# Performance work log

Hardware: AMD Instinct MI355X
Metric: run time of the kernel (lower is better)

Reference implementation:

```python
import jax, jax.numpy as jnp
import numpy as np

T = 22        # TypeEncoder.tensor_size() (assumed)
H = 2         # attention heads
C = 64        # hc_graph (per-head out channels)
L = 3         # num_hops
LEAFCAT = 5   # len(LeafType.valid_categories()) (assumed)
NSIZES = 8    # len(LeafType.valid_sizes()) (assumed)
HL = 64       # hc_linear
HT = 64       # hc_task == hc_leafsize
SLOPE = 0.2   # PyG GATConv negative_slope


def _gat(x, src, dst, W, asrc, adst, b):
    # PyG GATConv (concat=True, dropout=0, self-loops already appended to src/dst)
    N = x.shape[0]
    h = (x @ W).reshape(N, H, C)                      # [N,H,C]
    a_s = jnp.einsum('nhc,hc->nh', h, asrc)            # per-node src score
    a_d = jnp.einsum('nhc,hc->nh', h, adst)            # per-node dst score
    e = jax.nn.leaky_relu(a_s[src] + a_d[dst], SLOPE)  # [E+N,H]
    m = jax.ops.segment_max(e, dst, num_segments=N)
    p = jnp.exp(e - m[dst])
    s = jax.ops.segment_sum(p, dst, num_segments=N)
    alpha = p / (s[dst] + 1e-16)                       # scatter-softmax over in-edges
    out = jax.ops.segment_sum(h[src] * alpha[:, :, None], dst, num_segments=N)
    return out.reshape(N, H * C) + b


def _mlp2(z, W1, b1, W2, b2):
    return jax.nn.relu(z @ W1 + b1) @ W2 + b2


def setup_inputs() -> dict:
    key = jax.random.key(0)
    ks = jax.random.split(key, 32)
    N, E, NG, NPG = 102400, 1228800, 256, 400
    D = H * C
    g = lambda k, shp, fan: (jax.random.normal(k, shp, jnp.float32) / np.sqrt(fan)).astype(jnp.float32)
    z = lambda *shp: jnp.zeros(shp, jnp.float32)
    return {
        'x': jax.random.normal(ks[0], (N, D), jnp.float32),
        'edge_index': jax.random.randint(ks[1], (2, E), 0, N),
        'batch': jnp.repeat(jnp.arange(NG, dtype=jnp.int32), NPG),
        'gat_W': g(ks[2], (L, D, D), D),
        'gat_asrc': g(ks[3], (L, H, C), C),
        'gat_adst': g(ks[4], (L, H, C), C),
        'gat_b': z(L, D),
        'shared_W': g(ks[5], (D + T, HL), D + T),
        'shared_b': z(HL),
        'ptr_W1': g(ks[6], (3, HL, HT), HL), 'ptr_b1': z(3, HT),
        'ptr_W2': g(ks[7], (3, HT, 3), HT), 'ptr_b2': z(3, 3),
        'cat_W1': g(ks[8], (HL, HT), HL), 'cat_b1': z(HT),
        'cat_W2': g(ks[9], (HT, LEAFCAT), HT), 'cat_b2': z(LEAFCAT),
        'sf_W1': g(ks[10], (2, HL, HT), HL), 'sf_b1': z(2, HT),
        'sf_W2': g(ks[11], (2, HT, 1), HT), 'sf_b2': z(2, 1),
        'bool_W1': g(ks[12], (HL + T + LEAFCAT + 2, HT), HL + T + LEAFCAT + 2), 'bool_b1': z(HT),
        'bool_W2': g(ks[13], (HT, 1), HT), 'bool_b2': z(1),
        'size_W1': g(ks[14], (HL + T + LEAFCAT + 3, HT), HL + T + LEAFCAT + 3), 'size_b1': z(HT),
        'size_W2': g(ks[15], (HT, NSIZES), HT), 'size_b2': z(NSIZES),
    }


def reference(x, edge_index, batch, gat_W, gat_asrc, gat_adst, gat_b,
              shared_W, shared_b, ptr_W1, ptr_b1, ptr_W2, ptr_b2,
              cat_W1, cat_b1, cat_W2, cat_b2, sf_W1, sf_b1, sf_W2, sf_b2,
              bool_W1, bool_b1, bool_W2, bool_b2, size_W1, size_b1, size_W2, size_b2):
    N = x.shape[0]
    num_graphs = int(batch[-1]) + 1                    # batch is sorted per-graph ids
    node0 = jnp.searchsorted(batch, jnp.arange(num_graphs))  # first node of each graph
    dtype_vec = x[node0, :T]                           # NodeEncoder.split_node_vec dtype slice
    loops = jnp.arange(N)
    src = jnp.concatenate([edge_index[0], loops])      # GATConv add_self_loops=True
    dst = jnp.concatenate([edge_index[1], loops])
    h = x
    for l in range(L):
        h = _gat(h, src, dst, gat_W[l], gat_asrc[l], gat_adst[l], gat_b[l])
        if l < L - 1:
            h = jax.nn.relu(h)
    zf = jax.nn.relu(jnp.concatenate([h[node0], dtype_vec], axis=1) @ shared_W + shared_b)
    # 3 pointer heads, batched
    p = jax.nn.relu(jnp.einsum('gh,khd->kgd', zf, ptr_W1) + ptr_b1[:, None, :])
    ptr = jnp.einsum('kgd,kdo->kgo', p, ptr_W2) + ptr_b2[:, None, :]
    cat_logits = _mlp2(zf, cat_W1, cat_b1, cat_W2, cat_b2)
    q = jax.nn.relu(jnp.einsum('gh,khd->kgd', zf, sf_W1) + sf_b1[:, None, :])
    sf = jnp.einsum('kgd,kdo->kgo', q, sf_W2) + sf_b2[:, None, :]
    signed, floating = sf[0], sf[1]
    bool_in = jnp.concatenate([zf, dtype_vec, cat_logits, signed, floating], axis=1)
    bool_logit = _mlp2(bool_in, bool_W1, bool_b1, bool_W2, bool_b2)
    size_in = jnp.concatenate([bool_in, bool_logit], axis=1)
    size_logits = _mlp2(size_in, size_W1, size_b1, size_W2, size_b2)
    return (ptr[0], ptr[1], ptr[2], cat_logits, signed, floating, bool_logit, size_logits)
```

## Files before the change

### kernel.cpp

```cpp
#include <hip/hip_runtime.h>
#include <hip/hip_bf16.h>

typedef __hip_bfloat16 bf16;
typedef __attribute__((ext_vector_type(8))) short short8;
typedef __attribute__((ext_vector_type(4))) float floatx4;

#define MF(a, b, c) __builtin_amdgcn_mfma_f32_16x16x32_bf16(a, b, c, 0, 0, 0)

__device__ __forceinline__ float b2f(bf16 v) { return __bfloat162float(v); }
__device__ __forceinline__ unsigned short f2us(float f) {
    bf16 h = __float2bfloat16(f);
    return *(unsigned short*)&h;
}
__device__ __forceinline__ float lo2f(unsigned hv) { return __uint_as_float(hv << 16); }
__device__ __forceinline__ float hi2f(unsigned hv) { return __uint_as_float(hv & 0xffff0000u); }
__device__ __forceinline__ float leaky(float v) { return v > 0.f ? v : 0.2f * v; }

__device__ __forceinline__ float ldw(const void* p, size_t i, int f32) {
    return f32 ? ((const float*)p)[i] : b2f(((const bf16*)p)[i]);
}

template <int F32>
__device__ __forceinline__ float LDWt(const void* p, size_t i) {
    return F32 ? ((const float*)p)[i] : b2f(((const bf16*)p)[i]);
}

__device__ __forceinline__ int or16(const int* f) {
    int r = 0;
#pragma unroll
    for (int j = 0; j < 16; j++) r |= f[j];
    return r;
}

__device__ __forceinline__ void quadred(float part[4]) {
#pragma unroll
    for (int m = 1; m <= 8; m <<= 1)
#pragma unroll
        for (int r = 0; r < 4; r++) part[r] += __shfl_xor(part[r], m);
}

__global__ void k_detect_zero(const void* x, int* flagv, char* zbase, size_t zbytes) {
    int b = blockIdx.x;
    int t = threadIdx.x;
    if (b < 16) {
        __shared__ int sbad;
        if (t == 0) sbad = 0;
        __syncthreads();
        float v = b2f(((const bf16*)x)[b * 256 + t]);
        if (!(fabsf(v) < 1e10f)) sbad = 1;
        __syncthreads();
        if (t == 0) flagv[b] = sbad;
    } else {
        size_t off = (size_t)(b - 16) * 4096 + (size_t)t * 16;
        if (off < zbytes) *(uint4*)(zbase + off) = make_uint4(0u, 0u, 0u, 0u);
    }
}

__global__ void k_prep_fused(const void* __restrict__ x, unsigned short* __restrict__ Ab,
                             int nvec,
                             const void* __restrict__ gw, unsigned short* __restrict__ Wt,
                             const void* as_, const void* ad_, const void* b_,
                             float* asF, float* adF, float* bF,
                             const void* sW_, const void* pW1_, const void* cW1_,
                             const void* fW1_, const void* bW1_, const void* zW1_,
                             unsigned short* __restrict__ Whd,
                             const int* __restrict__ batch, int* __restrict__ node0,
                             unsigned char* __restrict__ rootb,
                             unsigned char* __restrict__ flag2, int N,
                             const int* __restrict__ flagv, int nbx8) {
    int b = blockIdx.x;
    int t = threadIdx.x;
    int f32 = or16(flagv);
    if (b < nbx8) {
        int i = b * 256 + t;
        if (i < nvec) {
            if (!f32) {
                ((uint4*)Ab)[i] = ((const uint4*)x)[i];
            } else {
                float4 a = ((const float4*)x)[2 * i];
                float4 c = ((const float4*)x)[2 * i + 1];
                uint4 o;
                o.x = ((unsigned)f2us(a.y) << 16) | f2us(a.x);
                o.y = ((unsigned)f2us(a.w) << 16) | f2us(a.z);
                o.z = ((unsigned)f2us(c.y) << 16) | f2us(c.x);
                o.w = ((unsigned)f2us(c.w) << 16) | f2us(c.z);
                ((uint4*)Ab)[i] = o;
            }
        }
    } else if (b < nbx8 + 192) {
        int i = (b - nbx8) * 256 + t;
        int l = i >> 14, rem = i & 16383, n = rem >> 7, k = rem & 127;
        Wt[i] = f2us(ldw(gw, (size_t)l * 16384 + (size_t)k * 128 + n, f32));
    } else if (b < nbx8 + 194) {
        int i = (b - nbx8 - 192) * 256 + t;
        if (i < 384) {
            asF[i] = ldw(as_, i, f32);
            adF[i] = ldw(ad_, i, f32);
            bF[i] = ldw(b_, i, f32);
        }
    } else if (b < nbx8 + 194 + 184) {
        int i = (b - nbx8 - 194) * 256 + t;
        float v;
        if (i < 10240) {
            int n = i / 160, k = i - n * 160;
            v = (k < 150) ? ldw(sW_, (size_t)k * 64 + n, f32) : 0.f;
        } else if (i < 22528) {
            int j = i - 10240;
            int kk = j >> 12, r = j & 4095, n = r >> 6, k = r & 63;
            v = ldw(pW1_, (size_t)kk * 4096 + (size_t)k * 64 + n, f32);
        } else if (i < 26624) {
            int j = i - 22528;
            int n = j >> 6, k = j & 63;
            v = ldw(cW1_, (size_t)k * 64 + n, f32);
        } else if (i < 34816) {
            int j = i - 26624;
            int kk = j >> 12, r = j & 4095, n = r >> 6, k = r & 63;
            v = ldw(fW1_, (size_t)kk * 4096 + (size_t)k * 64 + n, f32);
        } else if (i < 40960) {
            int j = i - 34816;
            int n = j / 96, k = j - n * 96;
            v = (k < 93) ? ldw(bW1_, (size_t)k * 64 + n, f32) : 0.f;
        } else {
            int j = i - 40960;
            int n = j / 96, k = j - n * 96;
            v = (k < 94) ? ldw(zW1_, (size_t)k * 64 + n, f32) : 0.f;
        }
        Whd[i] = f2us(v);
    } else {
        int i = (b - nbx8 - 194 - 184) * 256 + t;
        if (i < N) {
            int bb = batch[i];
            if (i == 0 || batch[i - 1] != bb) {
                node0[bb] = i;
                rootb[i] = 1;
                flag2[i] = 1;
            }
        }
    }
}

__global__ void k_scan3x(const int* __restrict__ counts,
                         const unsigned char* __restrict__ flag1,
                         const unsigned char* __restrict__ flag2,
                         int* __restrict__ offs, int* __restrict__ wp1, int* __restrict__ wp2,
                         int* __restrict__ bsums, int n) {
    __shared__ int s[256];
    int tid = threadIdx.x;
    int i = blockIdx.x * 256 + tid;
#pragma unroll
    for (int a = 0; a < 3; a++) {
        int v = 0;
        if (i < n) v = (a == 0) ? counts[i] : (a == 1) ? (int)flag1[i] : (int)flag2[i];
        s[tid] = v;
        __syncthreads();
        for (int d = 1; d < 256; d <<= 1) {
            int t2 = (tid >= d) ? s[tid - d] : 0;
            __syncthreads();
            s[tid] += t2;
            __syncthreads();
        }
        int incl = s[tid];
        if (i < n) {
            if (a == 0) offs[i] = incl - v;
            else if (a == 1) wp1[i] = incl - v;
            else wp2[i] = incl - v;
        }
        if (tid == 255) bsums[a * 512 + blockIdx.x] = incl;
        __syncthreads();
    }
}

__global__ void k_scan2x(int* __restrict__ bsums, int nb, int* __restrict__ nact) {
    __shared__ int s[512];
    int tid = threadIdx.x;
#pragma unroll
    for (int a = 0; a < 3; a++) {
        int* arr = bsums + a * 512;
        int v = (tid < nb) ? arr[tid] : 0;
        s[tid] = v;
        __syncthreads();
        for (int d = 1; d < 512; d <<= 1) {
            int t2 = (tid >= d) ? s[tid - d] : 0;
            __syncthreads();
            s[tid] += t2;
            __syncthreads();
        }
        arr[tid] = s[tid] - v;
        if (a >= 1 && tid == 511) nact[a - 1] = s[511];
        __syncthreads();
    }
}

__global__ void k_mark1(const int* __restrict__ ei, const unsigned char* __restrict__ flag2,
                        unsigned char* __restrict__ flag1, int E, int N, int eBlocks) {
    int b = blockIdx.x;
    if (b < eBlocks) {
        int e = b * 256 + threadIdx.x;
        if (e < E && flag2[ei[E + e]]) flag1[ei[e]] = 1;
    } else {
        int i = (b - eBlocks) * 256 + threadIdx.x;
        if (i < N && flag2[i]) flag1[i] = 1;
    }
}

__global__ void k_hist_masked(const int* __restrict__ ei, const unsigned char* __restrict__ flag1,
                              int* __restrict__ counts, int E) {
    int e = blockIdx.x * blockDim.x + threadIdx.x;
    if (e < E) {
        int d = ei[E + e];
        if (flag1[d]) atomicAdd(&counts[d], 1);
    }
}

__global__ void k_scatter_wl(const int* __restrict__ ei, const int* __restrict__ offs,
                             const int* __restrict__ bsums, int* __restrict__ cur,
                             const unsigned char* __restrict__ flag1,
                             const unsigned char* __restrict__ flag2,
                             const int* __restrict__ wp1, const int* __restrict__ wp2,
                             int* __restrict__ adj, int* __restrict__ wl1, int* __restrict__ wl2,
                             int E, int N, int eBlocks) {
    int b = blockIdx.x;
    if (b < eBlocks) {
        int e = b * 256 + threadIdx.x;
        if (e >= E) return;
        int d = ei[E + e];
        if (!flag1[d]) return;
        int r = atomicAdd(&cur[d], 1);
        adj[offs[d] + bsums[d >> 8] + r] = ei[e];
    } else {
        int i = (b - eBlocks) * 256 + threadIdx.x;
        if (i < N) {
            if (flag1[i]) wl1[wp1[i] + bsums[512 + (i >> 8)]] = i;
            if (flag2[i]) wl2[wp2[i] + bsums[1024 + (i >> 8)]] = i;
        }
    }
}

__device__ __forceinline__ void gemm_body(
    const unsigned short* __restrict__ Ab, const unsigned short* __restrict__ Wt,
    unsigned short* __restrict__ Bb, float4* __restrict__ asadv,
    const float* __restrict__ asF, const float* __restrict__ adF, int N,
    const int* __restrict__ wl, const int* __restrict__ nactp, int bb) {
    __shared__ __align__(16) unsigned short Ws[128 * 136];
    __shared__ __align__(16) unsigned short Cs[64 * 136];

    int t = threadIdx.x;
    int r0 = bb * 64;
    int nact = wl ? *nactp : N;
    if (r0 >= nact) return;

    {
        const uint4* src = (const uint4*)Wt;
#pragma unroll
        for (int k = 0; k < 8; k++) {
            int j = t + k * 256;
            int row = j >> 4, c16 = j & 15;
            *(uint4*)&Ws[row * 136 + c16 * 8] = src[j];
        }
    }
    __syncthreads();

    int lane = t & 63;
    int w = t >> 6;
    int ln = lane & 15;
    int quad = lane >> 4;

    int idx = r0 + w * 16 + ln;
    bool valid = idx < nact;
    int arow = idx < N ? idx : N - 1;
    if (wl) arow = valid ? wl[idx] : 0;
    bool wave_active = __any((int)valid);

    if (wave_active) {
        const unsigned short* ap = Ab + (size_t)arow * 128 + quad * 8;

        short8 afrag[4];
        if (valid) {
#pragma unroll
            for (int kt = 0; kt < 4; kt++)
                afrag[kt] = *(const short8*)(ap + kt * 32);
        } else {
#pragma unroll
            for (int kt = 0; kt < 4; kt++)
                afrag[kt] = (short8){0, 0, 0, 0, 0, 0, 0, 0};
        }

        floatx4 acc[8];
#pragma unroll
        for (int nt = 0; nt < 8; nt++) acc[nt] = (floatx4){0.f, 0.f, 0.f, 0.f};

#pragma unroll
        for (int nt = 0; nt < 8; nt++) {
            const unsigned short* wp = Ws + (nt * 16 + ln) * 136 + quad * 8;
#pragma unroll
            for (int kt = 0; kt < 4; kt++) {
                short8 bfrag = *(const short8*)(wp + kt * 32);
                acc[nt] = MF(afrag[kt], bfrag, acc[nt]);
            }
        }

        float as0[4] = {0, 0, 0, 0}, as1[4] = {0, 0, 0, 0};
        float ad0[4] = {0, 0, 0, 0}, ad1[4] = {0, 0, 0, 0};
#pragma unroll
        for (int nt = 0; nt < 8; nt++) {
            float asc = asF[nt * 16 + ln];
            float adc = adF[nt * 16 + ln];
#pragma unroll
            for (int r = 0; r < 4; r++) {
                float v = acc[nt][r];
                Cs[(w * 16 + quad * 4 + r) * 136 + nt * 16 + ln] = f2us(v);
                if (nt < 4) { as0[r] += v * asc; ad0[r] += v * adc; }
                else        { as1[r] += v * asc; ad1[r] += v * adc; }
            }
        }
#pragma unroll
        for (int mask = 1; mask <= 8; mask <<= 1) {
#pragma unroll
            for (int r = 0; r < 4; r++) {
                as0[r] += __shfl_xor(as0[r], mask);
                as1[r] += __shfl_xor(as1[r], mask);
                ad0[r] += __shfl_xor(ad0[r], mask);
                ad1[r] += __shfl_xor(ad1[r], mask);
            }
        }
        if (ln == 0) {
#pragma unroll
            for (int r = 0; r < 4; r++) {
                int idx3 = r0 + w * 16 + quad * 4 + r;
                if (idx3 < nact) {
                    int row = wl ? wl[idx3] : idx3;
                    asadv[row] = make_float4(as0[r], as1[r], ad0[r], ad1[r]);
                }
            }
        }
    }
    __syncthreads();

    {
        int idx2 = r0 + (t >> 2);
        int cseg = (t & 3) * 32;
        if (idx2 < nact) {
            int grow = wl ? wl[idx2] : idx2;
            const short8* srcp = (const short8*)&Cs[(t >> 2) * 136 + cseg];
            short8* dstp = (short8*)&Bb[(size_t)grow * 128 + cseg];
#pragma unroll
            for (int u = 0; u < 4; u++) dstp[u] = srcp[u];
        }
    }
}

__global__ __launch_bounds__(256) void k_gemm_mfma(
    const unsigned short* __restrict__ Ab, const unsigned short* __restrict__ Wt,
    unsigned short* __restrict__ Bb, float4* __restrict__ asadv,
    const float* __restrict__ asF, const float* __restrict__ adF, int N,
    const int* __restrict__ wl, const int* __restrict__ nactp) {
    gemm_body(Ab, Wt, Bb, asadv, asF, adF, N, wl, nactp, blockIdx.x);
}

__global__ __launch_bounds__(256) void k_gemm0_mark(
    const unsigned short* __restrict__ Ab, const unsigned short* __restrict__ Wt,
    unsigned short* __restrict__ Bb, float4* __restrict__ asadv,
    const float* __restrict__ asF, const float* __restrict__ adF, int N,
    const int* __restrict__ ei, const unsigned char* __restrict__ rootb,
    unsigned char* __restrict__ flag2, int E, int markBlocks) {
    int b = blockIdx.x;
    if (b < markBlocks) {
        int e = b * 256 + threadIdx.x;
        if (e < E) {
            int d = ei[E + e];
            if (rootb[d]) flag2[ei[e]] = 1;
        }
        return;
    }
    gemm_body(Ab, Wt, Bb, asadv, asF, adF, N, nullptr, nullptr, b - markBlocks);
}

__global__ void k_gat_agg(const uint2* __restrict__ Bu2, const float4* __restrict__ asadv,
                          const int* __restrict__ offs, const int* __restrict__ bsums,
                          const int* __restrict__ counts,
                          const int* __restrict__ adj, const float* __restrict__ biasF,
                          uint2* __restrict__ Au2, float2* __restrict__ pE,
                          const int* __restrict__ nactp, int nfix, int dorelu, int byidx,
                          const int* __restrict__ wl) {
    int wave = (blockIdx.x * blockDim.x + threadIdx.x) >> 6;
    int lane = threadIdx.x & 63;
    int hl = lane & 31;
    int hb = lane & 32;
    int idx = wave * 2 + (lane >> 5);
    int n = nfix ? nfix : *nactp;
    if (idx >= n) return;
    int node = wl[idx];
    int head = hl >> 4;

    float4 self = asadv[node];
    float ad0 = self.z, ad1 = self.w;
    float es0 = __expf(leaky(self.x + ad0));
    float es1 = __expf(leaky(self.y + ad1));

    int o = offs[node] + bsums[node >> 8];
    int c = counts[node];
    uint2 hvs = Bu2[(size_t)node * 32 + hl];
    float acc0, acc1, acc2, acc3;

    if (c <= 32) {
        int src_r = 0;
        float p0 = 0.f, p1 = 0.f;
        if (hl < c) {
            src_r = adj[o + hl];
            float4 av = asadv[src_r];
            p0 = __expf(leaky(av.x + ad0));
            p1 = __expf(leaky(av.y + ad1));
        }
        float t0 = p0, t1 = p1;
#pragma unroll
        for (int mask = 1; mask <= 16; mask <<= 1) {
            t0 += __shfl_xor(t0, mask);
            t1 += __shfl_xor(t1, mask);
        }
        float inv0 = 1.f / (es0 + t0 + 1e-16f);
        float inv1 = 1.f / (es1 + t1 + 1e-16f);
        p0 *= inv0;
        p1 *= inv1;
        float aself = head ? es1 * inv1 : es0 * inv0;
        acc0 = aself * lo2f(hvs.x);
        acc1 = aself * hi2f(hvs.x);
        acc2 = aself * lo2f(hvs.y);
        acc3 = aself * hi2f(hvs.y);

        uint2 hq[4];
#pragma unroll
        for (int j = 0; j < 4; j++) {
            int s2 = __shfl(src_r, hb + j);
            hq[j] = make_uint2(0u, 0u);
            if (j < c) hq[j] = Bu2[(size_t)s2 * 32 + hl];
        }

        for (int base = 0; base < c; base += 4) {
            uint2 cu[4];
            float av4[4];
#pragma unroll
            for (int j = 0; j < 4; j++) {
                cu[j] = hq[j];
                int idx2 = (base + j) & 31;
                float a0 = __shfl(p0, hb + idx2);
                float a1 = __shfl(p1, hb + idx2);
                float a = head ? a1 : a0;
                av4[j] = (base + j < c) ? a : 0.f;
            }
#pragma unroll
            for (int j = 0; j < 4; j++) {
                int nx = base + 4 + j;
                int s2 = __shfl(src_r, hb + (nx & 31));
                if (nx < c) hq[j] = Bu2[(size_t)s2 * 32 + hl];
            }
#pragma unroll
            for (int j = 0; j < 4; j++) {
                acc0 += av4[j] * lo2f(cu[j].x);
                acc1 += av4[j] * hi2f(cu[j].x);
                acc2 += av4[j] * lo2f(cu[j].y);
                acc3 += av4[j] * hi2f(cu[j].y);
            }
        }
    } else {
        float sum0 = es0, sum1 = es1;
        for (int base = 0; base < c; base += 32) {
            int i = base + hl;
            float p0 = 0.f, p1 = 0.f;
            if (i < c) {
                int s = adj[o + i];
                float4 av = asadv[s];
                p0 = __expf(leaky(av.x + ad0));
                p1 = __expf(leaky(av.y + ad1));
                pE[o + i] = make_float2(p0, p1);
            }
            float t0 = p0, t1 = p1;
#pragma unroll
            for (int mask = 1; mask <= 16; mask <<= 1) {
                t0 += __shfl_xor(t0, mask);
                t1 += __shfl_xor(t1, mask);
            }
            sum0 += t0; sum1 += t1;
        }
        float inv0 = 1.f / (sum0 + 1e-16f);
        float inv1 = 1.f / (sum1 + 1e-16f);
        float aself = head ? es1 * inv1 : es0 * inv0;
        float invh = head ? inv1 : inv0;
        acc0 = aself * lo2f(hvs.x);
        acc1 = aself * hi2f(hvs.x);
        acc2 = aself * lo2f(hvs.y);
        acc3 = aself * hi2f(hvs.y);
        for (int i = 0; i < c; i++) {
            int s = adj[o + i];
            float2 pp = pE[o + i];
            uint2 hv = Bu2[(size_t)s * 32 + hl];
            float a = (head ? pp.y : pp.x) * invh;
            acc0 += a * lo2f(hv.x);
            acc1 += a * hi2f(hv.x);
            acc2 += a * lo2f(hv.y);
            acc3 += a * hi2f(hv.y);
        }
    }

    float4 bb4 = ((const float4*)biasF)[hl];
    float q0 = acc0 + bb4.x;
    float q1 = acc1 + bb4.y;
    float q2 = acc2 + bb4.z;
    float q3 = acc3 + bb4.w;
    if (dorelu) {
        q0 = fmaxf(q0, 0.f); q1 = fmaxf(q1, 0.f);
        q2 = fmaxf(q2, 0.f); q3 = fmaxf(q3, 0.f);
    }
    Au2[(size_t)(byidx ? idx : node) * 32 + hl] =
        make_uint2(((unsigned)f2us(q1) << 16) | f2us(q0),
                   ((unsigned)f2us(q3) << 16) | f2us(q2));
}

template <int F32>
__device__ void heads_mfma_body(
    const unsigned* __restrict__ hroot32, const void* __restrict__ x,
    const int* __restrict__ node0, const unsigned short* __restrict__ Whd,
    const void* sb, const void* pb1, const void* pW2, const void* pb2,
    const void* cb1, const void* cW2, const void* cb2,
    const void* fb1, const void* fW2, const void* fb2,
    const void* bb1, const void* bW2, const void* bb2,
    const void* zb1, const void* zW2, const void* zb2,
    void* __restrict__ outv) {
    __shared__ __align__(16) unsigned short hinS[64 * 168];
    __shared__ __align__(16) unsigned short TwS[4][16 * 168];

    int t = threadIdx.x;
    int g0b = blockIdx.x * 64;
    bf16* outb = (bf16*)outv;
    float* outf = (float*)outv;
#define STORE(idx, val) do { if (F32) outf[idx] = (val); else outb[idx] = __float2bfloat16(val); } while (0)

    {
        unsigned* h32 = (unsigned*)hinS;
        for (int j = t; j < 64 * 64; j += 256) {
            int gl = j >> 6, c = j & 63;
            h32[gl * 84 + c] = hroot32[(size_t)(g0b + gl) * 64 + c];
        }
        for (int j = t; j < 64 * 20; j += 256) {
            int gl = j / 20, c = j - gl * 20;
            int n0 = node0[g0b + gl];
            int k0 = 2 * c;
            float d0 = (k0 < 22) ? LDWt<F32>(x, (size_t)n0 * 128 + k0) : 0.f;
            float d1 = (k0 + 1 < 22) ? LDWt<F32>(x, (size_t)n0 * 128 + k0 + 1) : 0.f;
            h32[gl * 84 + 64 + c] = ((unsigned)f2us(d1) << 16) | f2us(d0);
        }
    }
    __syncthreads();

    int w = t >> 6;
    int lane = t & 63;
    int ln = lane & 15, quad = lane >> 4;
    unsigned short* T = TwS[w];
    int gq = quad * 4;
    int gw0 = g0b + w * 16;

    for (int j = lane; j < 16 * 32; j += 64) {
        int gl = j >> 5, c = j & 31;
        T[gl * 168 + 64 + c] =
            (c < 22) ? hinS[(w * 16 + gl) * 168 + 128 + c] : (unsigned short)0;
    }

    short8 afA[5];
#pragma unroll
    for (int kt = 0; kt < 5; kt++)
        afA[kt] = *(const short8*)&hinS[(w * 16 + ln) * 168 + quad * 8 + kt * 32];
#pragma unroll
    for (int nt = 0; nt < 4; nt++) {
        floatx4 acc = (floatx4){0.f, 0.f, 0.f, 0.f};
        const unsigned short* bp = Whd + (nt * 16 + ln) * 160 + quad * 8;
#pragma unroll
        for (int kt = 0; kt < 5; kt++)
            acc = MF(afA[kt], *(const short8*)(bp + kt * 32), acc);
        float bias = LDWt<F32>(sb, nt * 16 + ln);
#pragma unroll
        for (int r = 0; r < 4; r++)
            T[(gq + r) * 168 + nt * 16 + ln] = f2us(fmaxf(acc[r] + bias, 0.f));
    }
    __syncthreads();

    short8 af20 = *(const short8*)&T[ln * 168 + quad * 8];
    short8 af21 = *(const short8*)&T[ln * 168 + quad * 8 + 32];

#pragma unroll
    for (int k = 0; k < 3; k++) {
        const unsigned short* Bw = Whd + 10240 + k * 4096;
        floatx4 acc[4];
#pragma unroll
        for (int nt = 0; nt < 4; nt++) {
            floatx4 a = (floatx4){0.f, 0.f, 0.f, 0.f};
            const unsigned short* bp = Bw + (nt * 16 + ln) * 64 + quad * 8;
            a = MF(af20, *(const short8*)bp, a);
            a = MF(af21, *(const short8*)(bp + 32), a);
            float b1 = LDWt<F32>(pb1, k * 64 + nt * 16 + ln);
#pragma unroll
            for (int r = 0; r < 4; r++) a[r] = fmaxf(a[r] + b1, 0.f);
            acc[nt] = a;
        }
#pragma unroll
        for (int o = 0; o < 3; o++) {
            float w2[4], part[4];
#pragma unroll
            for (int nt = 0; nt < 4; nt++)
                w2[nt] = LDWt<F32>(pW2, (size_t)k * 192 + (size_t)(nt * 16 + ln) * 3 + o);
#pragma unroll
            for (int r = 0; r < 4; r++)
                part[r] = acc[0][r] * w2[0] + acc[1][r] * w2[1] +
                          acc[2][r] * w2[2] + acc[3][r] * w2[3];
            quadred(part);
            if (ln == 0) {
                float b2 = LDWt<F32>(pb2, k * 3 + o);
#pragma unroll
                for (int r = 0; r < 4; r++)
                    STORE(k * 768 + (gw0 + gq + r) * 3 + o, part[r] + b2);
            }
        }
    }

    {
        const unsigned short* Bw = Whd + 22528;
        floatx4 acc[4];
#pragma unroll
        for (int nt = 0; nt < 4; nt++) {
            floatx4 a = (floatx4){0.f, 0.f, 0.f, 0.f};
            const unsigned short* bp = Bw + (nt * 16 + ln) * 64 + quad * 8;
            a = MF(af20, *(const short8*)bp, a);
            a = MF(af21, *(const short8*)(bp + 32), a);
            float b1 = LDWt<F32>(cb1, nt * 16 + ln);
#pragma unroll
            for (int r = 0; r < 4; r++) a[r] = fmaxf(a[r] + b1, 0.f);
            acc[nt] = a;
        }
#pragma unroll
        for (int o = 0; o < 5; o++) {
            float w2[4], part[4];
#pragma unroll
            for (int nt = 0; nt < 4; nt++)
                w2[nt] = LDWt<F32>(cW2, (size_t)(nt * 16 + ln) * 5 + o);
#pragma unroll
            for (int r = 0; r < 4; r++)
                part[r] = acc[0][r] * w2[0] + acc[1][r] * w2[1] +
                          acc[2][r] * w2[2] + acc[3][r] * w2[3];
            quadred(part);
            if (ln == 0) {
                float b2 = LDWt<F32>(cb2, o);
#pragma unroll
                for (int r = 0; r < 4; r++) {
                    float v = part[r] + b2;
                    T[(gq + r) * 168 + 86 + o] = f2us(v);
                    STORE(2304 + (gw0 + gq + r) * 5 + o, v);
                }
            }
        }
    }

#pragma unroll
    for (int k = 0; k < 2; k++) {
        const unsigned short* Bw = Whd + 26624 + k * 4096;
        floatx4 acc[4];
#pragma unroll
        for (int nt = 0; nt < 4; nt++) {
            floatx4 a = (floatx4){0.f, 0.f, 0.f, 0.f};
            const unsigned short* bp = Bw + (nt * 16 + ln) * 64 + quad * 8;
            a = MF(af20, *(const short8*)bp, a);
            a = MF(af21, *(const short8*)(bp + 32), a);
            float b1 = LDWt<F32>(fb1, k * 64 + nt * 16 + ln);
#pragma unroll
            for (int r = 0; r < 4; r++) a[r] = fmaxf(a[r] + b1, 0.f);
            acc[nt] = a;
        }
        float w2[4], part[4];
#pragma unroll
        for (int nt = 0; nt < 4; nt++)
            w2[nt] = LDWt<F32>(fW2, (size_t)k * 64 + nt * 16 + ln);
#pragma unroll
        for (int r = 0; r < 4; r++)
            part[r] = acc[0][r] * w2[0] + acc[1][r] * w2[1] +
                      acc[2][r] * w2[2] + acc[3][r] * w2[3];
        quadred(part);
        if (ln == 0) {
            float b2 = LDWt<F32>(fb2, k);
#pragma unroll
            for (int r = 0; r < 4; r++) {
                float v = part[r] + b2;
                T[(gq + r) * 168 + 91 + k] = f2us(v);
                STORE(3584 + k * 256 + (gw0 + gq + r), v);
            }
        }
    }
    __syncthreads();

    short8 af3 = *(const short8*)&T[ln * 168 + 64 + quad * 8];

    {
        const unsigned short* Bw = Whd + 34816;
        floatx4 acc[4];
#pragma unroll
        for (int nt = 0; nt < 4; nt++) {
            floatx4 a = (floatx4){0.f, 0.f, 0.f, 0.f};
            const unsigned short* bp = Bw + (nt * 16 + ln) * 96 + quad * 8;
            a = MF(af20, *(const short8*)bp, a);
            a = MF(af21, *(const short8*)(bp + 32), a);
            a = MF(af3, *(const short8*)(bp + 64), a);
            float b1 = LDWt<F32>(bb1, nt * 16 + ln);
#pragma unroll
            for (int r = 0; r < 4; r++) a[r] = fmaxf(a[r] + b1, 0.f);
            acc[nt] = a;
        }
        float w2[4], part[4];
#pragma unroll
        for (int nt = 0; nt < 4; nt++)
            w2[nt] = LDWt<F32>(bW2, nt * 16 + ln);
#pragma unroll
        for (int r = 0; r < 4; r++)
            part[r] = acc[0][r] * w2[0] + acc[1][r] * w2[1] +
                      acc[2][r] * w2[2] + acc[3][r] * w2[3];
        quadred(part);
        if (ln == 0) {
            float b2 = LDWt<F32>(bb2, 0);
#pragma unroll
            for (int r = 0; r < 4; r++) {
                float v = part[r] + b2;
                T[(gq + r) * 168 + 93] = f2us(v);
                STORE(4096 + (gw0 + gq + r), v);
            }
        }
    }
    __syncthreads();

    af3 = *(const short8*)&T[ln * 168 + 64 + quad * 8];

    {
        const unsigned short* Bw = Whd + 40960;
        floatx4 acc[4];
#pragma unroll
        for (int nt = 0; nt < 4; nt++) {
            floatx4 a = (floatx4){0.f, 0.f, 0.f, 0.f};
            const unsigned short* bp = Bw + (nt * 16 + ln) * 96 + quad * 8;
            a = MF(af20, *(const short8*)bp, a);
            a = MF(af21, *(const short8*)(bp + 32), a);
            a = MF(af3, *(const short8*)(bp + 64), a);
            float b1 = LDWt<F32>(zb1, nt * 16 + ln);
#pragma unroll
            for (int r = 0; r < 4; r++) a[r] = fmaxf(a[r] + b1, 0.f);
            acc[nt] = a;
        }
#pragma unroll
        for (int o = 0; o < 8; o++) {
            float w2[4], part[4];
#pragma unroll
            for (int nt = 0; nt < 4; nt++)
                w2[nt] = LDWt<F32>(zW2, (size_t)(nt * 16 + ln) * 8 + o);
#pragma unroll
            for (int r = 0; r < 4; r++)
                part[r] = acc[0][r] * w2[0] + acc[1][r] * w2[1] +
                          acc[2][r] * w2[2] + acc[3][r] * w2[3];
            quadred(part);
            if (ln == 0) {
                float b2 = LDWt<F32>(zb2, o);
#pragma unroll
                for (int r = 0; r < 4; r++)
                    STORE(4352 + (gw0 + gq + r) * 8 + o, part[r] + b2);
            }
        }
    }
#undef STORE
}

__global__ __launch_bounds__(256) void k_heads_mfma(
    const unsigned* __restrict__ hroot32, const void* __restrict__ x,
    const int* __restrict__ node0, const unsigned short* __restrict__ Whd,
    const void* sb, const void* pb1, const void* pW2, const void* pb2,
    const void* cb1, const void* cW2, const void* cb2,
    const void* fb1, const void* fW2, const void* fb2,
    const void* bb1, const void* bW2, const void* bb2,
    const void* zb1, const void* zW2, const void* zb2,
    void* __restrict__ outv, const int* __restrict__ flagv) {
    if (or16(flagv))
        heads_mfma_body<1>(hroot32, x, node0, Whd, sb, pb1, pW2, pb2, cb1, cW2, cb2,
                           fb1, fW2, fb2, bb1, bW2, bb2, zb1, zW2, zb2, outv);
    else
        heads_mfma_body<0>(hroot32, x, node0, Whd, sb, pb1, pW2, pb2, cb1, cW2, cb2,
                           fb1, fW2, fb2, bb1, bW2, bb2, zb1, zW2, zb2, outv);
}


extern "C" void kernel_launch(void* const* d_in, const int* in_sizes, int n_in,
                              void* d_out, int out_size, void* d_ws, size_t ws_size,
                              hipStream_t stream) {
    const void* x     = d_in[0];
    const int*  ei    = (const int*)d_in[1];
    const int*  batch = (const int*)d_in[2];

    int N = in_sizes[0] / 128;
    int E = in_sizes[1] / 2;

    char* w = (char*)d_ws;
    float4* asad = (float4*)w;              w += (size_t)N * 16;
    unsigned short* A = (unsigned short*)w; w += (size_t)N * 128 * 2;
    unsigned short* B = (unsigned short*)w; w += (size_t)N * 128 * 2;
    float2* pE = (float2*)w;                w += (size_t)E * 8;
    unsigned short* Wt = (unsigned short*)w; w += 3 * 16384 * 2;
    unsigned short* Whd = (unsigned short*)w; w += 47104 * 2;
    float* asF = (float*)w;                 w += 384 * 4;
    float* adF = (float*)w;                 w += 384 * 4;
    float* bF = (float*)w;                  w += 384 * 4;
    int* offs = (int*)w;                    w += (size_t)N * 4;
    int* wp1 = (int*)w;                     w += (size_t)N * 4;
    int* wp2 = (int*)w;                     w += (size_t)N * 4;
    int* wl1 = (int*)w;                     w += (size_t)N * 4;
    int* wl2 = (int*)w;                     w += (size_t)N * 4;
    int* adj = (int*)w;                     w += (size_t)E * 4;
    int* bsums = (int*)w;                   w += 3 * 512 * 4;
    int* node0 = (int*)w;                   w += 256 * 4;
    int* nact = (int*)w;                    w += 64;
    unsigned* hroot = (unsigned*)w;         w += 256 * 128 * 2;
    char* zbase = w;
    int* counts = (int*)w;                  w += (size_t)N * 4;
    int* cur = (int*)w;                     w += (size_t)N * 4;
    unsigned char* flag1 = (unsigned char*)w; w += (size_t)N;
    unsigned char* flag2 = (unsigned char*)w; w += (size_t)N;
    unsigned char* rootb = (unsigned char*)w; w += (size_t)N;
    size_t zbytes = (size_t)N * 11;
    int* flagv = (int*)w;                   w += 64;

    int nb = (N + 255) / 256;
    int nvec = N * 16;
    int nbx8 = (nvec + 255) / 256;
    int nbE = (E + 255) / 256;
    int gemmBlocks = (N + 63) / 64;
    int zBlocks = (int)((zbytes + 4095) / 4096);

    k_detect_zero<<<16 + zBlocks, 256, 0, stream>>>(x, flagv, zbase, zbytes);

    k_prep_fused<<<nbx8 + 194 + 184 + nb, 256, 0, stream>>>(
        x, A, nvec, d_in[3], Wt, d_in[4], d_in[5], d_in[6],
        asF, adF, bF,
        d_in[7], d_in[9], d_in[13], d_in[17], d_in[21], d_in[25], Whd,
        batch, node0, rootb, flag2, N, flagv, nbx8);

    k_gemm0_mark<<<nbE + gemmBlocks, 256, 0, stream>>>(
        A, Wt, B, asad, asF, adF, N, ei, rootb, flag2, E, nbE);

    k_mark1<<<nbE + nb, 256, 0, stream>>>(ei, flag2, flag1, E, N, nbE);

    k_hist_masked<<<nbE, 256, 0, stream>>>(ei, flag1, counts, E);

    k_scan3x<<<nb, 256, 0, stream>>>(counts, flag1, flag2, offs, wp1, wp2, bsums, N);
    k_scan2x<<<1, 512, 0, stream>>>(bsums, nb, nact);

    k_scatter_wl<<<nbE + nb, 256, 0, stream>>>(
        ei, offs, bsums, cur, flag1, flag2, wp1, wp2, adj, wl1, wl2, E, N, nbE);

    int nwaves = (N + 1) / 2;
    int aggblocks = (nwaves + 3) / 4;

    k_gat_agg<<<aggblocks, 256, 0, stream>>>(
        (const uint2*)B, asad, offs, bsums, counts, adj, bF, (uint2*)A, pE,
        nact, 0, 1, 0, wl1);

    k_gemm_mfma<<<gemmBlocks, 256, 0, stream>>>(
        A, Wt + 16384, B, asad, asF + 128, adF + 128, N, wl1, nact);
    k_gat_agg<<<aggblocks, 256, 0, stream>>>(
        (const uint2*)B, asad, offs, bsums, counts, adj, bF + 128, (uint2*)A, pE,
        nact + 1, 0, 1, 0, wl2);

    k_gemm_mfma<<<gemmBlocks, 256, 0, stream>>>(
        A, Wt + 2 * 16384, B, asad, asF + 256, adF + 256, N, wl2, nact + 1);

    k_gat_agg<<<32, 256, 0, stream>>>(
        (const uint2*)B, asad, offs, bsums, counts, adj, bF + 256, (uint2*)hroot, pE,
        nact, 256, 0, 1, node0);

    k_heads_mfma<<<4, 256, 0, stream>>>(
        hroot, x, node0, Whd,
        d_in[8], d_in[10], d_in[11], d_in[12],
        d_in[14], d_in[15], d_in[16],
        d_in[18], d_in[19], d_in[20],
        d_in[22], d_in[23], d_in[24],
        d_in[26], d_in[27], d_in[28],
        d_out, flagv);
}
```

Baseline: 316.4 us.

## Fuse CSR build phases into one cooperative kernel and skip bf16 input copy

Moves the root-marking into the zeroing kernel and each mark stage one launch earlier, so one launch is removed from the prefix chain. Histogram, block scan, top-level scan and scatter now run in a single cooperative grid-synced kernel, with the old multi-kernel path kept as a fallback. The first GEMM reads bf16 input directly instead of copying it into a staging buffer. The aim is to cut kernel launch gaps and one full copy of the node features, at the cost of grid-sync overhead and lower parallelism in the persistent kernel.

Measured after the change: 836.7 us. 2.64x slower.

```diff
diff --git a/kernel.cpp b/kernel.cpp
--- a/kernel.cpp
+++ b/kernel.cpp
@@ -1,5 +1,8 @@
 #include <hip/hip_runtime.h>
 #include <hip/hip_bf16.h>
+#include <hip/hip_cooperative_groups.h>
+
+namespace cg = cooperative_groups;
 
 typedef __hip_bfloat16 bf16;
 typedef __attribute__((ext_vector_type(8))) short short8;
@@ -39,7 +42,10 @@
         for (int r = 0; r < 4; r++) part[r] += __shfl_xor(part[r], m);
 }
 
-__global__ void k_detect_zero(const void* x, int* flagv, char* zbase, size_t zbytes) {
+__global__ void k_detect_zero(const void* x, int* flagv, char* zbase, size_t zbytes,
+                              const int* __restrict__ batch, int* __restrict__ node0,
+                              unsigned char* __restrict__ rootb,
+                              unsigned char* __restrict__ flag2, int N, int zBlocks) {
     int b = blockIdx.x;
     int t = threadIdx.x;
     if (b < 16) {
@@ -50,9 +56,18 @@
         if (!(fabsf(v) < 1e10f)) sbad = 1;
         __syncthreads();
         if (t == 0) flagv[b] = sbad;
-    } else {
+    } else if (b < 16 + zBlocks) {
         size_t off = (size_t)(b - 16) * 4096 + (size_t)t * 16;
         if (off < zbytes) *(uint4*)(zbase + off) = make_uint4(0u, 0u, 0u, 0u);
+    } else {
+        int i = (b - 16 - zBlocks) * 256 + t;
+        if (i < N) {
+            int bb = batch[i];
+            int isroot = (i == 0) || (batch[i - 1] != bb);
+            rootb[i] = (unsigned char)isroot;
+            flag2[i] = (unsigned char)isroot;
+            if (isroot) node0[bb] = i;
+        }
     }
 }
 
@@ -64,28 +79,24 @@
                              const void* sW_, const void* pW1_, const void* cW1_,
                              const void* fW1_, const void* bW1_, const void* zW1_,
                              unsigned short* __restrict__ Whd,
-                             const int* __restrict__ batch, int* __restrict__ node0,
-                             unsigned char* __restrict__ rootb,
-                             unsigned char* __restrict__ flag2, int N,
+                             const int* __restrict__ ei, const unsigned char* __restrict__ rootb,
+                             unsigned char* __restrict__ flag2, int E,
                              const int* __restrict__ flagv, int nbx8) {
     int b = blockIdx.x;
     int t = threadIdx.x;
     int f32 = or16(flagv);
     if (b < nbx8) {
+        if (!f32) return;
         int i = b * 256 + t;
         if (i < nvec) {
-            if (!f32) {
-                ((uint4*)Ab)[i] = ((const uint4*)x)[i];
-            } else {
-                float4 a = ((const float4*)x)[2 * i];
-                float4 c = ((const float4*)x)[2 * i + 1];
-                uint4 o;
-                o.x = ((unsigned)f2us(a.y) << 16) | f2us(a.x);
-                o.y = ((unsigned)f2us(a.w) << 16) | f2us(a.z);
-                o.z = ((unsigned)f2us(c.y) << 16) | f2us(c.x);
-                o.w = ((unsigned)f2us(c.w) << 16) | f2us(c.z);
-                ((uint4*)Ab)[i] = o;
-            }
+            float4 a = ((const float4*)x)[2 * i];
+            float4 c = ((const float4*)x)[2 * i + 1];
+            uint4 o;
+            o.x = ((unsigned)f2us(a.y) << 16) | f2us(a.x);
+            o.y = ((unsigned)f2us(a.w) << 16) | f2us(a.z);
+            o.z = ((unsigned)f2us(c.y) << 16) | f2us(c.x);
+            o.w = ((unsigned)f2us(c.w) << 16) | f2us(c.z);
+            ((uint4*)Ab)[i] = o;
         }
     } else if (b < nbx8 + 192) {
         int i = (b - nbx8) * 256 + t;
@@ -127,15 +138,104 @@
         }
         Whd[i] = f2us(v);
     } else {
-        int i = (b - nbx8 - 194 - 184) * 256 + t;
-        if (i < N) {
-            int bb = batch[i];
-            if (i == 0 || batch[i - 1] != bb) {
-                node0[bb] = i;
-                rootb[i] = 1;
-                flag2[i] = 1;
-            }
-        }
+        int e = (b - nbx8 - 194 - 184) * 256 + t;
+        if (e < E && rootb[ei[E + e]]) flag2[ei[e]] = 1;
+    }
+}
+
+__global__ void k_build(const int* __restrict__ ei,
+                        const unsigned char* __restrict__ flag1,
+                        const unsigned char* __restrict__ flag2,
+                        int* __restrict__ counts, int* __restrict__ offs,
+                        int* __restrict__ wp1, int* __restrict__ wp2,
+                        int* __restrict__ bsums, int* __restrict__ nact,
+                        int* __restrict__ cur, int* __restrict__ adj,
+                        int* __restrict__ wl1, int* __restrict__ wl2,
+                        int E, int N, int nb) {
+    cg::grid_group grid = cg::this_grid();
+    __shared__ int s[512];
+    int t = threadIdx.x;
+    int gsz = gridDim.x * 256;
+    int gid0 = blockIdx.x * 256 + t;
+
+    for (int e = gid0; e < E; e += gsz) {
+        int d = ei[E + e];
+        if (flag1[d]) atomicAdd(&counts[d], 1);
+    }
+    __threadfence();
+    grid.sync();
+
+    for (int chunk = blockIdx.x; chunk < nb; chunk += gridDim.x) {
+        int i = chunk * 256 + t;
+#pragma unroll
+        for (int a = 0; a < 3; a++) {
+            int v = 0;
+            if (i < N) v = (a == 0) ? counts[i] : (a == 1) ? (int)flag1[i] : (int)flag2[i];
+            s[t] = v;
+            __syncthreads();
+            for (int d = 1; d < 256; d <<= 1) {
+                int t2 = (t >= d) ? s[t - d] : 0;
+                __syncthreads();
+                s[t] += t2;
+                __syncthreads();
+            }
+            int incl = s[t];
+            if (i < N) {
+                if (a == 0) offs[i] = incl - v;
+                else if (a == 1) wp1[i] = incl - v;
+                else wp2[i] = incl - v;
+            }
+            if (t == 255) bsums[a * 512 + chunk] = incl;
+            __syncthreads();
+        }
+    }
+    __threadfence();
+    grid.sync();
+
+    if (blockIdx.x == 0) {
+#pragma unroll
+        for (int a = 0; a < 3; a++) {
+            int* arr = bsums + a * 512;
+            int v0 = (t < nb) ? arr[t] : 0;
+            int v1 = (t + 256 < nb) ? arr[t + 256] : 0;
+            s[t] = v0;
+            s[t + 256] = v1;
+            __syncthreads();
+            for (int d = 1; d < 512; d <<= 1) {
+                int a0 = (t >= d) ? s[t - d] : 0;
+                int a1 = (t + 256 >= d) ? s[t + 256 - d] : 0;
+                __syncthreads();
+                s[t] += a0;
+                s[t + 256] += a1;
+                __syncthreads();
+            }
+            arr[t] = s[t] - v0;
+            arr[t + 256] = s[t + 256] - v1;
+            if (a >= 1 && t == 255) nact[a - 1] = s[511];
+            __syncthreads();
+        }
+    }
+    __threadfence();
+    grid.sync();
+
+    for (int e = gid0; e < E; e += gsz) {
+        int d = ei[E + e];
+        if (!flag1[d]) continue;
+        int r = atomicAdd(&cur[d], 1);
+        adj[offs[d] + bsums[d >> 8] + r] = ei[e];
+    }
+    for (int i = gid0; i < N; i += gsz) {
+        if (flag1[i]) wl1[wp1[i] + bsums[512 + (i >> 8)]] = i;
+        if (flag2[i]) wl2[wp2[i] + bsums[1024 + (i >> 8)]] = i;
+    }
+}
+
+__global__ void k_hist_masked(const int* __restrict__ ei, const unsigned char* __restrict__ flag1,
+                              int* __restrict__ counts, int E) {
+    int e = blockIdx.x * blockDim.x + threadIdx.x;
+    if (e < E) {
+        int d = ei[E + e];
+        if (flag1[d]) atomicAdd(&counts[d], 1);
     }
 }
 
@@ -188,27 +288,6 @@
         arr[tid] = s[tid] - v;
         if (a >= 1 && tid == 511) nact[a - 1] = s[511];
         __syncthreads();
-    }
-}
-
-__global__ void k_mark1(const int* __restrict__ ei, const unsigned char* __restrict__ flag2,
-                        unsigned char* __restrict__ flag1, int E, int N, int eBlocks) {
-    int b = blockIdx.x;
-    if (b < eBlocks) {
-        int e = b * 256 + threadIdx.x;
-        if (e < E && flag2[ei[E + e]]) flag1[ei[e]] = 1;
-    } else {
-        int i = (b - eBlocks) * 256 + threadIdx.x;
-        if (i < N && flag2[i]) flag1[i] = 1;
-    }
-}
-
-__global__ void k_hist_masked(const int* __restrict__ ei, const unsigned char* __restrict__ flag1,
-                              int* __restrict__ counts, int E) {
-    int e = blockIdx.x * blockDim.x + threadIdx.x;
-    if (e < E) {
-        int d = ei[E + e];
-        if (flag1[d]) atomicAdd(&counts[d], 1);
     }
 }
 
@@ -237,7 +316,7 @@
 }
 
 __device__ __forceinline__ void gemm_body(
-    const unsigned short* __restrict__ Ab, const unsigned short* __restrict__ Wt,
+    const unsigned short* __restrict__ Asrc, const unsigned short* __restrict__ Wt,
     unsigned short* __restrict__ Bb, float4* __restrict__ asadv,
     const float* __restrict__ asF, const float* __restrict__ adF, int N,
     const int* __restrict__ wl, const int* __restrict__ nactp, int bb) {
@@ -272,7 +351,7 @@
     bool wave_active = __any((int)valid);
 
     if (wave_active) {
-        const unsigned short* ap = Ab + (size_t)arow * 128 + quad * 8;
+        const unsigned short* ap = Asrc + (size_t)arow * 128 + quad * 8;
 
         short8 afrag[4];
         if (valid) {
@@ -358,21 +437,26 @@
 }
 
 __global__ __launch_bounds__(256) void k_gemm0_mark(
-    const unsigned short* __restrict__ Ab, const unsigned short* __restrict__ Wt,
+    const unsigned short* __restrict__ Ab, const void* __restrict__ xraw,
+    const unsigned short* __restrict__ Wt,
     unsigned short* __restrict__ Bb, float4* __restrict__ asadv,
     const float* __restrict__ asF, const float* __restrict__ adF, int N,
-    const int* __restrict__ ei, const unsigned char* __restrict__ rootb,
-    unsigned char* __restrict__ flag2, int E, int markBlocks) {
+    const int* __restrict__ ei, const unsigned char* __restrict__ flag2,
+    unsigned char* __restrict__ flag1, int E, int markE, int markN,
+    const int* __restrict__ flagv) {
     int b = blockIdx.x;
-    if (b < markBlocks) {
+    if (b < markE) {
         int e = b * 256 + threadIdx.x;
-        if (e < E) {
-            int d = ei[E + e];
-            if (rootb[d]) flag2[ei[e]] = 1;
-        }
+        if (e < E && flag2[ei[E + e]]) flag1[ei[e]] = 1;
         return;
     }
-    gemm_body(Ab, Wt, Bb, asadv, asF, adF, N, nullptr, nullptr, b - markBlocks);
+    if (b < markE + markN) {
+        int i = (b - markE) * 256 + threadIdx.x;
+        if (i < N && flag2[i]) flag1[i] = 1;
+        return;
+    }
+    const unsigned short* Asrc = or16(flagv) ? Ab : (const unsigned short*)xraw;
+    gemm_body(Asrc, Wt, Bb, asadv, asF, adF, N, nullptr, nullptr, b - markE - markN);
 }
 
 __global__ void k_gat_agg(const uint2* __restrict__ Bu2, const float4* __restrict__ asadv,
@@ -822,10 +906,10 @@
     int* counts = (int*)w;                  w += (size_t)N * 4;
     int* cur = (int*)w;                     w += (size_t)N * 4;
     unsigned char* flag1 = (unsigned char*)w; w += (size_t)N;
+    size_t zbytes = (size_t)N * 9;
+    int* flagv = (int*)w;                   w += 64;
+    unsigned char* rootb = (unsigned char*)w; w += (size_t)N;
     unsigned char* flag2 = (unsigned char*)w; w += (size_t)N;
-    unsigned char* rootb = (unsigned char*)w; w += (size_t)N;
-    size_t zbytes = (size_t)N * 11;
-    int* flagv = (int*)w;                   w += 64;
 
     int nb = (N + 255) / 256;
     int nvec = N * 16;
@@ -834,26 +918,53 @@
     int gemmBlocks = (N + 63) / 64;
     int zBlocks = (int)((zbytes + 4095) / 4096);
 
-    k_detect_zero<<<16 + zBlocks, 256, 0, stream>>>(x, flagv, zbase, zbytes);
-
-    k_prep_fused<<<nbx8 + 194 + 184 + nb, 256, 0, stream>>>(
+    k_detect_zero<<<16 + zBlocks + nb, 256, 0, stream>>>(
+        x, flagv, zbase, zbytes, batch, node0, rootb, flag2, N, zBlocks);
+
+    k_prep_fused<<<nbx8 + 194 + 184 + nbE, 256, 0, stream>>>(
         x, A, nvec, d_in[3], Wt, d_in[4], d_in[5], d_in[6],
         asF, adF, bF,
         d_in[7], d_in[9], d_in[13], d_in[17], d_in[21], d_in[25], Whd,
-        batch, node0, rootb, flag2, N, flagv, nbx8);
-
-    k_gemm0_mark<<<nbE + gemmBlocks, 256, 0, stream>>>(
-        A, Wt, B, asad, asF, adF, N, ei, rootb, flag2, E, nbE);
-
-    k_mark1<<<nbE + nb, 256, 0, stream>>>(ei, flag2, flag1, E, N, nbE);
-
-    k_hist_masked<<<nbE, 256, 0, stream>>>(ei, flag1, counts, E);
-
-    k_scan3x<<<nb, 256, 0, stream>>>(counts, flag1, flag2, offs, wp1, wp2, bsums, N);
-    k_scan2x<<<1, 512, 0, stream>>>(bsums, nb, nact);
-
-    k_scatter_wl<<<nbE + nb, 256, 0, stream>>>(
-        ei, offs, bsums, cur, flag1, flag2, wp1, wp2, adj, wl1, wl2, E, N, nbE);
+        ei, rootb, flag2, E, flagv, nbx8);
+
+    k_gemm0_mark<<<nbE + nb + gemmBlocks, 256, 0, stream>>>(
+        A, x, Wt, B, asad, asF, adF, N, ei, flag2, flag1, E, nbE, nb, flagv);
+
+    {
+        static int coopBlocks = -1;
+        if (coopBlocks < 0) {
+            int dev = 0, coopOK = 0, perCU = 0;
+            hipGetDevice(&dev);
+            hipDeviceGetAttribute(&coopOK, hipDeviceAttributeCooperativeLaunch, dev);
+            if (coopOK &&
+                hipOccupancyMaxActiveBlocksPerMultiprocessor(&perCU, (const void*)k_build, 256, 0) == hipSuccess &&
+                perCU > 0) {
+                int cap = perCU * 256;
+                coopBlocks = cap < 1024 ? cap : 1024;
+            } else {
+                coopBlocks = 0;
+            }
+        }
+        bool done = false;
+        if (coopBlocks > 0) {
+            void* args[] = {(void*)&ei, (void*)&flag1, (void*)&flag2, (void*)&counts,
+                            (void*)&offs, (void*)&wp1, (void*)&wp2, (void*)&bsums,
+                            (void*)&nact, (void*)&cur, (void*)&adj, (void*)&wl1,
+                            (void*)&wl2, (void*)&E, (void*)&N, (void*)&nb};
+            hipError_t err = hipLaunchCooperativeKernel((const void*)k_build,
+                                                        dim3(coopBlocks), dim3(256),
+                                                        args, 0, stream);
+            if (err == hipSuccess) done = true;
+            else coopBlocks = 0;
+        }
+        if (!done) {
+            k_hist_masked<<<nbE, 256, 0, stream>>>(ei, flag1, counts, E);
+            k_scan3x<<<nb, 256, 0, stream>>>(counts, flag1, flag2, offs, wp1, wp2, bsums, N);
+            k_scan2x<<<1, 512, 0, stream>>>(bsums, nb, nact);
+            k_scatter_wl<<<nbE + nb, 256, 0, stream>>>(
+                ei, offs, bsums, cur, flag1, flag2, wp1, wp2, adj, wl1, wl2, E, N, nbE);
+        }
+    }
 
     int nwaves = (N + 1) / 2;
     int aggblocks = (nwaves + 3) / 4;
```

## Fold root marking into zeroing kernel, skip bf16 copy, merge mark1 into gemm0

Applied to the files above, without the earlier changes.

Root detection moves into the first zeroing/detection kernel, and rootb and flag2 are now written explicitly instead of being zeroed. This lets the first edge-marking pass run inside prep_fused and the second pass run alongside the layer-0 GEMM. The GEMM reads x directly when the input is already bf16, which removes the full N×128 copy into A. One kernel launch and a large memory copy are removed, at the cost of more branching inside the fused kernels.

Result: no change. 316.3 us (-0.0%).

```diff
diff --git a/kernel.cpp b/kernel.cpp
--- a/kernel.cpp
+++ b/kernel.cpp
@@ -39,7 +39,10 @@
         for (int r = 0; r < 4; r++) part[r] += __shfl_xor(part[r], m);
 }
 
-__global__ void k_detect_zero(const void* x, int* flagv, char* zbase, size_t zbytes) {
+__global__ void k_detect_zero(const void* x, int* flagv, char* zbase, size_t zbytes,
+                              const int* __restrict__ batch, int* __restrict__ node0,
+                              unsigned char* __restrict__ rootb,
+                              unsigned char* __restrict__ flag2, int N, int zBlocks) {
     int b = blockIdx.x;
     int t = threadIdx.x;
     if (b < 16) {
@@ -50,9 +53,18 @@
         if (!(fabsf(v) < 1e10f)) sbad = 1;
         __syncthreads();
         if (t == 0) flagv[b] = sbad;
-    } else {
+    } else if (b < 16 + zBlocks) {
         size_t off = (size_t)(b - 16) * 4096 + (size_t)t * 16;
         if (off < zbytes) *(uint4*)(zbase + off) = make_uint4(0u, 0u, 0u, 0u);
+    } else {
+        int i = (b - 16 - zBlocks) * 256 + t;
+        if (i < N) {
+            int bb = batch[i];
+            int isroot = (i == 0) || (batch[i - 1] != bb);
+            rootb[i] = (unsigned char)isroot;
+            flag2[i] = (unsigned char)isroot;
+            if (isroot) node0[bb] = i;
+        }
     }
 }
 
@@ -64,28 +76,24 @@
                              const void* sW_, const void* pW1_, const void* cW1_,
                              const void* fW1_, const void* bW1_, const void* zW1_,
                              unsigned short* __restrict__ Whd,
-                             const int* __restrict__ batch, int* __restrict__ node0,
-                             unsigned char* __restrict__ rootb,
-                             unsigned char* __restrict__ flag2, int N,
+                             const int* __restrict__ ei, const unsigned char* __restrict__ rootb,
+                             unsigned char* __restrict__ flag2, int E,
                              const int* __restrict__ flagv, int nbx8) {
     int b = blockIdx.x;
     int t = threadIdx.x;
     int f32 = or16(flagv);
     if (b < nbx8) {
+        if (!f32) return;
         int i = b * 256 + t;
         if (i < nvec) {
-            if (!f32) {
-                ((uint4*)Ab)[i] = ((const uint4*)x)[i];
-            } else {
-                float4 a = ((const float4*)x)[2 * i];
-                float4 c = ((const float4*)x)[2 * i + 1];
-                uint4 o;
-                o.x = ((unsigned)f2us(a.y) << 16) | f2us(a.x);
-                o.y = ((unsigned)f2us(a.w) << 16) | f2us(a.z);
-                o.z = ((unsigned)f2us(c.y) << 16) | f2us(c.x);
-                o.w = ((unsigned)f2us(c.w) << 16) | f2us(c.z);
-                ((uint4*)Ab)[i] = o;
-            }
+            float4 a = ((const float4*)x)[2 * i];
+            float4 c = ((const float4*)x)[2 * i + 1];
+            uint4 o;
+            o.x = ((unsigned)f2us(a.y) << 16) | f2us(a.x);
+            o.y = ((unsigned)f2us(a.w) << 16) | f2us(a.z);
+            o.z = ((unsigned)f2us(c.y) << 16) | f2us(c.x);
+            o.w = ((unsigned)f2us(c.w) << 16) | f2us(c.z);
+            ((uint4*)Ab)[i] = o;
         }
     } else if (b < nbx8 + 192) {
         int i = (b - nbx8) * 256 + t;
@@ -127,15 +135,17 @@
         }
         Whd[i] = f2us(v);
     } else {
-        int i = (b - nbx8 - 194 - 184) * 256 + t;
-        if (i < N) {
-            int bb = batch[i];
-            if (i == 0 || batch[i - 1] != bb) {
-                node0[bb] = i;
-                rootb[i] = 1;
-                flag2[i] = 1;
-            }
-        }
+        int e = (b - nbx8 - 194 - 184) * 256 + t;
+        if (e < E && rootb[ei[E + e]]) flag2[ei[e]] = 1;
+    }
+}
+
+__global__ void k_hist_masked(const int* __restrict__ ei, const unsigned char* __restrict__ flag1,
+                              int* __restrict__ counts, int E) {
+    int e = blockIdx.x * blockDim.x + threadIdx.x;
+    if (e < E) {
+        int d = ei[E + e];
+        if (flag1[d]) atomicAdd(&counts[d], 1);
     }
 }
 
@@ -188,27 +198,6 @@
         arr[tid] = s[tid] - v;
         if (a >= 1 && tid == 511) nact[a - 1] = s[511];
         __syncthreads();
-    }
-}
-
-__global__ void k_mark1(const int* __restrict__ ei, const unsigned char* __restrict__ flag2,
-                        unsigned char* __restrict__ flag1, int E, int N, int eBlocks) {
-    int b = blockIdx.x;
-    if (b < eBlocks) {
-        int e = b * 256 + threadIdx.x;
-        if (e < E && flag2[ei[E + e]]) flag1[ei[e]] = 1;
-    } else {
-        int i = (b - eBlocks) * 256 + threadIdx.x;
-        if (i < N && flag2[i]) flag1[i] = 1;
-    }
-}
-
-__global__ void k_hist_masked(const int* __restrict__ ei, const unsigned char* __restrict__ flag1,
-                              int* __restrict__ counts, int E) {
-    int e = blockIdx.x * blockDim.x + threadIdx.x;
-    if (e < E) {
-        int d = ei[E + e];
-        if (flag1[d]) atomicAdd(&counts[d], 1);
     }
 }
 
@@ -237,7 +226,7 @@
 }
 
 __device__ __forceinline__ void gemm_body(
-    const unsigned short* __restrict__ Ab, const unsigned short* __restrict__ Wt,
+    const unsigned short* __restrict__ Asrc, const unsigned short* __restrict__ Wt,
     unsigned short* __restrict__ Bb, float4* __restrict__ asadv,
     const float* __restrict__ asF, const float* __restrict__ adF, int N,
     const int* __restrict__ wl, const int* __restrict__ nactp, int bb) {
@@ -272,7 +261,7 @@
     bool wave_active = __any((int)valid);
 
     if (wave_active) {
-        const unsigned short* ap = Ab + (size_t)arow * 128 + quad * 8;
+        const unsigned short* ap = Asrc + (size_t)arow * 128 + quad * 8;
 
         short8 afrag[4];
         if (valid) {
@@ -358,21 +347,26 @@
 }
 
 __global__ __launch_bounds__(256) void k_gemm0_mark(
-    const unsigned short* __restrict__ Ab, const unsigned short* __restrict__ Wt,
+    const unsigned short* __restrict__ Ab, const void* __restrict__ xraw,
+    const unsigned short* __restrict__ Wt,
     unsigned short* __restrict__ Bb, float4* __restrict__ asadv,
     const float* __restrict__ asF, const float* __restrict__ adF, int N,
-    const int* __restrict__ ei, const unsigned char* __restrict__ rootb,
-    unsigned char* __restrict__ flag2, int E, int markBlocks) {
+    const int* __restrict__ ei, const unsigned char* __restrict__ flag2,
+    unsigned char* __restrict__ flag1, int E, int markE, int markN,
+    const int* __restrict__ flagv) {
     int b = blockIdx.x;
-    if (b < markBlocks) {
+    if (b < markE) {
         int e = b * 256 + threadIdx.x;
-        if (e < E) {
-            int d = ei[E + e];
-            if (rootb[d]) flag2[ei[e]] = 1;
-        }
+        if (e < E && flag2[ei[E + e]]) flag1[ei[e]] = 1;
         return;
     }
-    gemm_body(Ab, Wt, Bb, asadv, asF, adF, N, nullptr, nullptr, b - markBlocks);
+    if (b < markE + markN) {
+        int i = (b - markE) * 256 + threadIdx.x;
+        if (i < N && flag2[i]) flag1[i] = 1;
+        return;
+    }
+    const unsigned short* Asrc = or16(flagv) ? Ab : (const unsigned short*)xraw;
+    gemm_body(Asrc, Wt, Bb, asadv, asF, adF, N, nullptr, nullptr, b - markE - markN);
 }
 
 __global__ void k_gat_agg(const uint2* __restrict__ Bu2, const float4* __restrict__ asadv,
@@ -822,10 +816,10 @@
     int* counts = (int*)w;                  w += (size_t)N * 4;
     int* cur = (int*)w;                     w += (size_t)N * 4;
     unsigned char* flag1 = (unsigned char*)w; w += (size_t)N;
+    size_t zbytes = (size_t)N * 9;
+    int* flagv = (int*)w;                   w += 64;
+    unsigned char* rootb = (unsigned char*)w; w += (size_t)N;
     unsigned char* flag2 = (unsigned char*)w; w += (size_t)N;
-    unsigned char* rootb = (unsigned char*)w; w += (size_t)N;
-    size_t zbytes = (size_t)N * 11;
-    int* flagv = (int*)w;                   w += 64;
 
     int nb = (N + 255) / 256;
     int nvec = N * 16;
@@ -834,24 +828,21 @@
     int gemmBlocks = (N + 63) / 64;
     int zBlocks = (int)((zbytes + 4095) / 4096);
 
-    k_detect_zero<<<16 + zBlocks, 256, 0, stream>>>(x, flagv, zbase, zbytes);
-
-    k_prep_fused<<<nbx8 + 194 + 184 + nb, 256, 0, stream>>>(
+    k_detect_zero<<<16 + zBlocks + nb, 256, 0, stream>>>(
+        x, flagv, zbase, zbytes, batch, node0, rootb, flag2, N, zBlocks);
+
+    k_prep_fused<<<nbx8 + 194 + 184 + nbE, 256, 0, stream>>>(
         x, A, nvec, d_in[3], Wt, d_in[4], d_in[5], d_in[6],
         asF, adF, bF,
         d_in[7], d_in[9], d_in[13], d_in[17], d_in[21], d_in[25], Whd,
-        batch, node0, rootb, flag2, N, flagv, nbx8);
-
-    k_gemm0_mark<<<nbE + gemmBlocks, 256, 0, stream>>>(
-        A, Wt, B, asad, asF, adF, N, ei, rootb, flag2, E, nbE);
-
-    k_mark1<<<nbE + nb, 256, 0, stream>>>(ei, flag2, flag1, E, N, nbE);
+        ei, rootb, flag2, E, flagv, nbx8);
+
+    k_gemm0_mark<<<nbE + nb + gemmBlocks, 256, 0, stream>>>(
+        A, x, Wt, B, asad, asF, adF, N, ei, flag2, flag1, E, nbE, nb, flagv);
 
     k_hist_masked<<<nbE, 256, 0, stream>>>(ei, flag1, counts, E);
-
     k_scan3x<<<nb, 256, 0, stream>>>(counts, flag1, flag2, offs, wp1, wp2, bsums, N);
     k_scan2x<<<1, 512, 0, stream>>>(bsums, nb, nact);
-
     k_scatter_wl<<<nbE + nb, 256, 0, stream>>>(
         ei, offs, bsums, cur, flag1, flag2, wp1, wp2, adj, wl1, wl2, E, N, nbE);
 
```
